# Performance work log

Hardware: AMD Instinct MI355X
Metric: run time of the kernel (lower is better)

## Reference

```python
import jax, jax.numpy as jnp
import numpy as np

NEG_SLOPE = 0.2
EPS = 1e-16


def gatv2_conv(x, src, dst, n_nodes, Wl, Wr, att, bias):
    """GATv2Conv, heads=1, add_self_loops handled by caller via src/dst.
    x: [N, Fin]; src/dst: [E] (message j->i means src=j, dst=i).
    Wl, Wr: [Fin, Fout]; att: [Fout]; bias: [Fout].
    """
    xl = x @ Wl  # [N, Fout] (source transform)
    xr = x @ Wr  # [N, Fout] (target transform)
    # per-edge attention logit: a^T LeakyReLU(xl[j] + xr[i])
    h = xl[src] + xr[dst]                      # [E, Fout]
    e = jax.nn.leaky_relu(h, NEG_SLOPE) @ att  # [E]
    # segment softmax over incoming edges of each dst node
    m = jax.ops.segment_max(e, dst, num_segments=n_nodes)   # [N]
    ex = jnp.exp(e - m[dst])                                 # [E]
    denom = jax.ops.segment_sum(ex, dst, num_segments=n_nodes)  # [N]
    alpha = ex / (denom[dst] + EPS)                          # [E]
    # scatter-aggregate weighted source messages
    out = jax.ops.segment_sum(alpha[:, None] * xl[src], dst, num_segments=n_nodes)
    return out + bias


def glorot(key, shape):
    lim = np.sqrt(6.0 / (shape[0] + shape[1]))
    return jax.random.uniform(key, shape, jnp.float32, -lim, lim)


def setup_inputs() -> dict:
    key = jax.random.key(0)
    ks = jax.random.split(key, 9)
    N, E, Fin, H, Fout = 50000, 800000, 128, 64, 2
    x = jax.random.normal(ks[0], (N, Fin), jnp.float32)
    edge_index = jax.random.randint(ks[1], (2, E), 0, N, jnp.int64)
    return {
        "x": x,
        "edge_index": edge_index,
        "Wl1": glorot(ks[2], (Fin, H)),
        "Wr1": glorot(ks[3], (Fin, H)),
        "att1": glorot(ks[4], (H, 1))[:, 0],
        "b1": jnp.zeros((H,), jnp.float32),
        "Wl2": glorot(ks[5], (H, Fout)),
        "Wr2": glorot(ks[6], (H, Fout)),
        "att2": glorot(ks[7], (Fout, 1))[:, 0],
        "b2": jnp.zeros((Fout,), jnp.float32),
    }


def reference(x, edge_index, Wl1, Wr1, att1, b1, Wl2, Wr2, att2, b2):
    n_nodes = x.shape[0]
    # PyG GATv2Conv adds self-loops by default
    loops = jnp.arange(n_nodes, dtype=edge_index.dtype)
    src = jnp.concatenate([edge_index[0], loops])
    dst = jnp.concatenate([edge_index[1], loops])
    # eval mode: dropout is identity; the initial relu/dropout result is dead code
    h = gatv2_conv(x, src, dst, n_nodes, Wl1, Wr1, att1, b1)
    out = gatv2_conv(h, src, dst, n_nodes, Wl2, Wr2, att2, b2)
    return out
```

## Files before the change

### kernel.cpp

```cpp
#include <hip/hip_runtime.h>
#include <math.h>

#define FIN 128
#define H 64
#define FOUT 2
#define NEG_SLOPE 0.2f
#define EPS 1e-16f

#define SCAN_CHUNK 2048

typedef __attribute__((ext_vector_type(8))) short s8v;
typedef __attribute__((ext_vector_type(4))) float f4v;

__device__ __forceinline__ void load_bs(const int* __restrict__ blocksum, int nscan,
                                        int* bs, int tid){
  if(tid < 64){
    int v = (tid < nscan)? blocksum[tid] : 0;
    int incl = v;
    #pragma unroll
    for(int o=1;o<64;o<<=1){ int u=__shfl_up(incl,o); if(tid>=o) incl+=u; }
    bs[tid] = incl - v;
  }
  __syncthreads();
}

__global__ void k_prep(int* __restrict__ deg, int N, int ZB,
                       const float* __restrict__ Wl, const float* __restrict__ Wr,
                       unsigned short* __restrict__ pWh, unsigned short* __restrict__ pWe){
  int b = blockIdx.x;
  if(b < ZB){
    int i = b*256 + threadIdx.x;
    if(i < N) deg[i] = 0;
    return;
  }
  int idx = (b - ZB)*256 + threadIdx.x;
  int lane = idx & 63;
  int ctk  = idx >> 6;
  int k0   = (ctk & 3) * 32;
  int ct   = ctk >> 2;
  int c    = ct*16 + (lane & 15);
  int kb   = k0 + (lane >> 4)*8;
  const float* Wp = (c < 64) ? (Wl + c) : (Wr + (c - 64));
  #pragma unroll
  for(int j=0;j<8;j++){
    float v = Wp[(size_t)(kb + j)*H];
    unsigned u = __float_as_uint(v);
    unsigned short hb = (unsigned short)(u >> 16);
    float hv = __uint_as_float(((unsigned)hb) << 16);
    float ev = v - hv;
    unsigned short eb = (unsigned short)(__float_as_uint(ev) >> 16);
    pWh[(size_t)idx*8 + j] = hb;
    pWe[(size_t)idx*8 + j] = eb;
  }
}

__global__ __launch_bounds__(256) void k_gemm_deg(
    const float* __restrict__ x,
    const unsigned short* __restrict__ pWh, const unsigned short* __restrict__ pWe,
    float* __restrict__ xl, float* __restrict__ xr,
    unsigned short* __restrict__ xlb, int N, int GG,
    const int* __restrict__ ei, int E, int Etot,
    int* __restrict__ deg, int* __restrict__ rank){
  int tid = threadIdx.x;
  if((int)blockIdx.x >= GG){
    int i0 = (((int)blockIdx.x - GG)*256 + tid)*8;
    if(i0 >= Etot) return;
    if(i0 + 8 <= E && (E & 3) == 0){
      int4 da = *(const int4*)(ei + E + i0);
      int4 db = *(const int4*)(ei + E + i0 + 4);
      int r0 = atomicAdd(&deg[da.x],1);
      int r1 = atomicAdd(&deg[da.y],1);
      int r2 = atomicAdd(&deg[da.z],1);
      int r3 = atomicAdd(&deg[da.w],1);
      int r4 = atomicAdd(&deg[db.x],1);
      int r5 = atomicAdd(&deg[db.y],1);
      int r6 = atomicAdd(&deg[db.z],1);
      int r7 = atomicAdd(&deg[db.w],1);
      *(int4*)(rank + i0)     = make_int4(r0,r1,r2,r3);
      *(int4*)(rank + i0 + 4) = make_int4(r4,r5,r6,r7);
    } else if(i0 >= E && i0 + 8 <= Etot){
      int v = i0 - E;
      int r0 = atomicAdd(&deg[v+0],1);
      int r1 = atomicAdd(&deg[v+1],1);
      int r2 = atomicAdd(&deg[v+2],1);
      int r3 = atomicAdd(&deg[v+3],1);
      int r4 = atomicAdd(&deg[v+4],1);
      int r5 = atomicAdd(&deg[v+5],1);
      int r6 = atomicAdd(&deg[v+6],1);
      int r7 = atomicAdd(&deg[v+7],1);
      *(int4*)(rank + i0)     = make_int4(r0,r1,r2,r3);
      *(int4*)(rank + i0 + 4) = make_int4(r4,r5,r6,r7);
    } else {
      #pragma unroll
      for(int q=0;q<8;q++){
        int i = i0+q; if(i>=Etot) break;
        int dst = (i<E) ? ei[E+i] : (i-E);
        rank[i] = atomicAdd(&deg[dst],1);
      }
    }
    return;
  }

  int lane = tid & 63, wid = tid >> 6;
  int rowbase = blockIdx.x*64 + wid*16;
  int r = lane & 15, g = lane >> 4;

  int arow = rowbase + r; if(arow > N-1) arow = N-1;
  const float* xrow = x + (size_t)arow*FIN;

  s8v ah[4], ae[4];
  #pragma unroll
  for(int k0=0;k0<4;k0++){
    float4 va = *(const float4*)(xrow + k0*32 + g*8);
    float4 vb = *(const float4*)(xrow + k0*32 + g*8 + 4);
    float xs_[8] = {va.x,va.y,va.z,va.w,vb.x,vb.y,vb.z,vb.w};
    #pragma unroll
    for(int j=0;j<8;j++){
      unsigned u = __float_as_uint(xs_[j]);
      unsigned short hb = (unsigned short)(u >> 16);
      ah[k0][j] = (short)hb;
      float ev = xs_[j] - __uint_as_float(((unsigned)hb) << 16);
      ae[k0][j] = (short)(unsigned short)(__float_as_uint(ev) >> 16);
    }
  }

  #pragma unroll 2
  for(int ct=0;ct<8;ct++){
    f4v a = (f4v){0.f,0.f,0.f,0.f};
    #pragma unroll
    for(int k0=0;k0<4;k0++){
      size_t boff = ((size_t)(ct*4 + k0)*64 + lane)*8;
      s8v bh = *(const s8v*)(pWh + boff);
      s8v be = *(const s8v*)(pWe + boff);
      a = __builtin_amdgcn_mfma_f32_16x16x32_bf16(ah[k0], bh, a, 0,0,0);
      a = __builtin_amdgcn_mfma_f32_16x16x32_bf16(ah[k0], be, a, 0,0,0);
      a = __builtin_amdgcn_mfma_f32_16x16x32_bf16(ae[k0], bh, a, 0,0,0);
    }
    float* dst = (ct < 4) ? xl : xr;
    int cc = (ct & 3)*16 + r;
    #pragma unroll
    for(int rr=0;rr<4;rr++){
      int row = rowbase + g*4 + rr;
      if(row < N){
        dst[(size_t)row*H + cc] = a[rr];
        if(ct < 4){
          unsigned u = __float_as_uint(a[rr]);
          xlb[(size_t)row*H + cc] = (unsigned short)((u + 0x7FFF + ((u>>16)&1)) >> 16);
        }
      }
    }
  }
}

__global__ __launch_bounds__(256) void k_scan_a(const int* __restrict__ deg, int n,
                                                int* __restrict__ rowptr,
                                                int* __restrict__ blocksum){
  __shared__ int wsum[4];
  int tid = threadIdx.x, lane = tid & 63, wid = tid >> 6;
  int idx = blockIdx.x*SCAN_CHUNK + tid*8;
  int v[8];
  if(idx + 8 <= n){
    int4 a = *(const int4*)(deg + idx);
    int4 b = *(const int4*)(deg + idx + 4);
    v[0]=a.x;v[1]=a.y;v[2]=a.z;v[3]=a.w;v[4]=b.x;v[5]=b.y;v[6]=b.z;v[7]=b.w;
  } else {
    #pragma unroll
    for(int i=0;i<8;i++) v[i] = (idx+i<n)? deg[idx+i] : 0;
  }
  int pre[8]; int st=0;
  #pragma unroll
  for(int i=0;i<8;i++){ pre[i]=st; st+=v[i]; }
  int incl = st;
  #pragma unroll
  for(int o=1;o<64;o<<=1){ int u=__shfl_up(incl,o); if(lane>=o) incl+=u; }
  if(lane==63) wsum[wid]=incl;
  __syncthreads();
  if(tid==0){ int accu=0; for(int i=0;i<4;i++){ int t=wsum[i]; wsum[i]=accu; accu+=t; } }
  __syncthreads();
  int toff = wsum[wid] + incl - st;
  if(idx + 8 <= n){
    int4 o0 = make_int4(toff+pre[0],toff+pre[1],toff+pre[2],toff+pre[3]);
    int4 o1 = make_int4(toff+pre[4],toff+pre[5],toff+pre[6],toff+pre[7]);
    *(int4*)(rowptr+idx)=o0; *(int4*)(rowptr+idx+4)=o1;
  } else {
    #pragma unroll
    for(int i=0;i<8;i++) if(idx+i<n) rowptr[idx+i]=toff+pre[i];
  }
  if(tid==255){
    blocksum[blockIdx.x] = toff + st;
    if(blockIdx.x == gridDim.x-1) rowptr[n] = toff + st;
  }
}

__global__ void k_fill(const int* __restrict__ ei, int E, int Etot,
                       const int* __restrict__ rowptr,
                       const int* __restrict__ blocksum, int nscan,
                       const int* __restrict__ rank, int* __restrict__ csr_src){
  __shared__ int bs[64];
  int tid = threadIdx.x;
  load_bs(blocksum, nscan, bs, tid);
  int i0 = (blockIdx.x*blockDim.x + tid)*8;
  if(i0 >= Etot) return;
  if(i0 + 8 <= E && (E & 3) == 0){
    int4 sa = *(const int4*)(ei + i0);
    int4 sb = *(const int4*)(ei + i0 + 4);
    int4 da = *(const int4*)(ei + E + i0);
    int4 db = *(const int4*)(ei + E + i0 + 4);
    int4 ra = *(const int4*)(rank + i0);
    int4 rb = *(const int4*)(rank + i0 + 4);
    csr_src[rowptr[da.x] + bs[da.x>>11] + ra.x] = sa.x;
    csr_src[rowptr[da.y] + bs[da.y>>11] + ra.y] = sa.y;
    csr_src[rowptr[da.z] + bs[da.z>>11] + ra.z] = sa.z;
    csr_src[rowptr[da.w] + bs[da.w>>11] + ra.w] = sa.w;
    csr_src[rowptr[db.x] + bs[db.x>>11] + rb.x] = sb.x;
    csr_src[rowptr[db.y] + bs[db.y>>11] + rb.y] = sb.y;
    csr_src[rowptr[db.z] + bs[db.z>>11] + rb.z] = sb.z;
    csr_src[rowptr[db.w] + bs[db.w>>11] + rb.w] = sb.w;
  } else if(i0 >= E && i0 + 8 <= Etot){
    int4 ra = *(const int4*)(rank + i0);
    int4 rb = *(const int4*)(rank + i0 + 4);
    int v = i0 - E;
    csr_src[rowptr[v+0] + bs[(v+0)>>11] + ra.x] = v+0;
    csr_src[rowptr[v+1] + bs[(v+1)>>11] + ra.y] = v+1;
    csr_src[rowptr[v+2] + bs[(v+2)>>11] + ra.z] = v+2;
    csr_src[rowptr[v+3] + bs[(v+3)>>11] + ra.w] = v+3;
    csr_src[rowptr[v+4] + bs[(v+4)>>11] + rb.x] = v+4;
    csr_src[rowptr[v+5] + bs[(v+5)>>11] + rb.y] = v+5;
    csr_src[rowptr[v+6] + bs[(v+6)>>11] + rb.z] = v+6;
    csr_src[rowptr[v+7] + bs[(v+7)>>11] + rb.w] = v+7;
  } else {
    #pragma unroll
    for(int q=0;q<8;q++){
      int i = i0+q; if(i>=Etot) break;
      int src, dst;
      if(i<E){ src = ei[i]; dst = ei[E+i]; } else { src = i-E; dst = i-E; }
      csr_src[rowptr[dst] + bs[dst>>11] + rank[i]] = src;
    }
  }
}

__global__ void k_node1f(const int* __restrict__ rowptr, const int* __restrict__ blocksum,
                         int nscan, const int* __restrict__ csr_src,
                         const unsigned short* __restrict__ xlb, const float* __restrict__ xr,
                         const float* __restrict__ att, const float* __restrict__ b1,
                         const float* __restrict__ Wl2, const float* __restrict__ Wr2,
                         float* __restrict__ xl2, float* __restrict__ xr2, int N){
  __shared__ int bs[64];
  int tid = threadIdx.x;
  load_bs(blocksum, nscan, bs, tid);
  int node = blockIdx.x*8 + (tid>>5);
  int half = (tid >> 4) & 1;
  int gl = tid & 15;
  if(node >= N) return;
  int f4 = gl*4;
  float4 attv = *(const float4*)(att + f4);
  float4 xrv  = *(const float4*)(xr + (size_t)node*H + f4);
  int s = rowptr[node]   + bs[node>>11];
  int t = rowptr[node+1] + bs[(node+1)>>11];
  float d = 0.f;
  float ax=0.f, ay=0.f, az=0.f, aw=0.f;

  for(int k = s + half*8; k < t; k += 16){
    int tl = t - 1;
    int ks[8]; float4 xv[8]; float msk[8];
    #pragma unroll
    for(int j=0;j<8;j++){
      int kj = k + j;
      ks[j] = (kj < t) ? kj : tl;
      msk[j] = (kj < t) ? 1.f : 0.f;
    }
    int ss[8];
    #pragma unroll
    for(int j=0;j<8;j++) ss[j] = csr_src[ks[j]];
    #pragma unroll
    for(int j=0;j<8;j++){
      ushort4 uv = *(const ushort4*)(xlb + (size_t)ss[j]*H + f4);
      xv[j].x = __uint_as_float((unsigned)uv.x << 16);
      xv[j].y = __uint_as_float((unsigned)uv.y << 16);
      xv[j].z = __uint_as_float((unsigned)uv.z << 16);
      xv[j].w = __uint_as_float((unsigned)uv.w << 16);
    }
    #pragma unroll
    for(int j=0;j<8;j++){
      float h0 = xv[j].x + xrv.x, h1 = xv[j].y + xrv.y;
      float h2 = xv[j].z + xrv.z, h3 = xv[j].w + xrv.w;
      float l0 = (h0>0.f)? h0 : NEG_SLOPE*h0;
      float l1 = (h1>0.f)? h1 : NEG_SLOPE*h1;
      float l2 = (h2>0.f)? h2 : NEG_SLOPE*h2;
      float l3 = (h3>0.f)? h3 : NEG_SLOPE*h3;
      float e = l0*attv.x + l1*attv.y + l2*attv.z + l3*attv.w;
      #pragma unroll
      for(int o=1;o<16;o<<=1) e += __shfl_xor(e,o);
      float w = msk[j] * __expf(e);
      d  += w;
      ax += w*xv[j].x; ay += w*xv[j].y; az += w*xv[j].z; aw += w*xv[j].w;
    }
  }

  d  += __shfl_xor(d,16);
  ax += __shfl_xor(ax,16); ay += __shfl_xor(ay,16);
  az += __shfl_xor(az,16); aw += __shfl_xor(aw,16);

  float inv = 1.f/(d + EPS);
  float4 bv = *(const float4*)(b1 + f4);
  float h0 = ax*inv + bv.x, h1 = ay*inv + bv.y;
  float h2 = az*inv + bv.z, h3 = aw*inv + bv.w;
  const float* Wp = half ? Wr2 : Wl2;
  float pa = h0*Wp[(f4+0)*FOUT+0] + h1*Wp[(f4+1)*FOUT+0] + h2*Wp[(f4+2)*FOUT+0] + h3*Wp[(f4+3)*FOUT+0];
  float pb = h0*Wp[(f4+0)*FOUT+1] + h1*Wp[(f4+1)*FOUT+1] + h2*Wp[(f4+2)*FOUT+1] + h3*Wp[(f4+3)*FOUT+1];
  #pragma unroll
  for(int o=1;o<16;o<<=1){
    pa += __shfl_xor(pa,o); pb += __shfl_xor(pb,o);
  }
  if(gl==0){
    float2 pv = make_float2(pa,pb);
    if(half==0) *(float2*)(xl2 + node*2) = pv;
    else        *(float2*)(xr2 + node*2) = pv;
  }
}

__global__ void k_node2(const int* __restrict__ rowptr, const int* __restrict__ blocksum,
                        int nscan, const int* __restrict__ csr_src,
                        const float* __restrict__ xl2, const float* __restrict__ xr2,
                        const float* __restrict__ att2, const float* __restrict__ b2,
                        float* __restrict__ out, int N){
  __shared__ int bs[64];
  int tid = threadIdx.x;
  load_bs(blocksum, nscan, bs, tid);
  int node = blockIdx.x*16 + (tid>>4);
  int gl = tid & 15;
  if(node >= N) return;
  int s = rowptr[node]   + bs[node>>11];
  int t = rowptr[node+1] + bs[(node+1)>>11];
  float2 xrv = *(const float2*)(xr2 + node*2);
  float a0 = att2[0], a1 = att2[1];
  float den=0.f, n0=0.f, n1=0.f;
  for(int k=s+gl; k<t; k+=16){
    int src = csr_src[k];
    float2 xs = *(const float2*)(xl2 + src*2);
    float h0 = xs.x + xrv.x, h1 = xs.y + xrv.y;
    float l0 = (h0>0.f)? h0 : NEG_SLOPE*h0;
    float l1 = (h1>0.f)? h1 : NEG_SLOPE*h1;
    float ex = __expf(l0*a0 + l1*a1);
    den += ex; n0 += ex*xs.x; n1 += ex*xs.y;
  }
  #pragma unroll
  for(int o=1;o<16;o<<=1){
    den += __shfl_xor(den,o);
    n0  += __shfl_xor(n0,o);
    n1  += __shfl_xor(n1,o);
  }
  if(gl==0){
    float inv = 1.f/(den + EPS);
    out[node*2+0] = n0*inv + b2[0];
    out[node*2+1] = n1*inv + b2[1];
  }
}

extern "C" void kernel_launch(void* const* d_in, const int* in_sizes, int n_in,
                              void* d_out, int out_size, void* d_ws, size_t ws_size,
                              hipStream_t stream){
  const float* x    = (const float*)d_in[0];
  const int*   ei   = (const int*)d_in[1];
  const float* Wl1  = (const float*)d_in[2];
  const float* Wr1  = (const float*)d_in[3];
  const float* att1 = (const float*)d_in[4];
  const float* b1   = (const float*)d_in[5];
  const float* Wl2  = (const float*)d_in[6];
  const float* Wr2  = (const float*)d_in[7];
  const float* att2 = (const float*)d_in[8];
  const float* b2   = (const float*)d_in[9];
  int N = in_sizes[0]/FIN;
  int E = in_sizes[1]/2;
  int Etot = E + N;
  int nscan = (N + SCAN_CHUNK - 1) / SCAN_CHUNK;
  int noct  = (Etot + 7) / 8;
  int ZB = (N + 255) / 256;
  int GG = (N + 63) / 64;
  int GDO = (noct + 255) / 256;

  char* w = (char*)d_ws;
  size_t off = 0;
  auto alloc = [&](size_t bytes)->void*{
    void* p = w + off;
    off = (off + bytes + 255) & ~(size_t)255;
    return p;
  };
  float* xl1     = (float*)alloc((size_t)N*H*4);
  float* xr1     = (float*)alloc((size_t)N*H*4);
  unsigned short* xlb = (unsigned short*)alloc((size_t)N*H*2);
  int*   csr_src = (int*)  alloc((size_t)Etot*4);
  int*   rank    = (int*)  alloc((size_t)Etot*4);
  int*   deg     = (int*)  alloc((size_t)N*4);
  int*   rowptr  = (int*)  alloc((size_t)(N+1)*4);
  int*   blocksum= (int*)  alloc((size_t)64*4);
  float* xl2     = (float*)alloc((size_t)N*2*4);
  float* xr2     = (float*)alloc((size_t)N*2*4);
  unsigned short* pWh = (unsigned short*)alloc((size_t)2048*8*2);
  unsigned short* pWe = (unsigned short*)alloc((size_t)2048*8*2);

  k_prep<<<ZB+8, 256, 0, stream>>>(deg, N, ZB, Wl1, Wr1, pWh, pWe);
  k_gemm_deg<<<GG+GDO, 256, 0, stream>>>(x, pWh, pWe, xl1, xr1, xlb, N, GG,
                                         ei, E, Etot, deg, rank);
  k_scan_a<<<nscan,256,0,stream>>>(deg, N, rowptr, blocksum);
  k_fill<<<GDO,256,0,stream>>>(ei, E, Etot, rowptr, blocksum, nscan, rank, csr_src);
  k_node1f<<<(N+7)/8, 256, 0, stream>>>(rowptr, blocksum, nscan, csr_src,
                                        xlb, xr1, att1, b1, Wl2, Wr2, xl2, xr2, N);
  k_node2<<<(N+15)/16, 256, 0, stream>>>(rowptr, blocksum, nscan, csr_src,
                                         xl2, xr2, att2, b2, (float*)d_out, N);
}
```

Before: 122.1 us.

## Split GEMM and degree kernels, drop fp32 xl store, transpose MFMA for vector stores

```diff
diff --git a/kernel.cpp b/kernel.cpp
--- a/kernel.cpp
+++ b/kernel.cpp
@@ -54,61 +54,20 @@
   }
 }
 
-__global__ __launch_bounds__(256) void k_gemm_deg(
+__global__ __launch_bounds__(256) void k_gemm_mfma(
     const float* __restrict__ x,
     const unsigned short* __restrict__ pWh, const unsigned short* __restrict__ pWe,
-    float* __restrict__ xl, float* __restrict__ xr,
-    unsigned short* __restrict__ xlb, int N, int GG,
-    const int* __restrict__ ei, int E, int Etot,
-    int* __restrict__ deg, int* __restrict__ rank){
+    float* __restrict__ xr, unsigned short* __restrict__ xlb, int N){
   int tid = threadIdx.x;
-  if((int)blockIdx.x >= GG){
-    int i0 = (((int)blockIdx.x - GG)*256 + tid)*8;
-    if(i0 >= Etot) return;
-    if(i0 + 8 <= E && (E & 3) == 0){
-      int4 da = *(const int4*)(ei + E + i0);
-      int4 db = *(const int4*)(ei + E + i0 + 4);
-      int r0 = atomicAdd(&deg[da.x],1);
-      int r1 = atomicAdd(&deg[da.y],1);
-      int r2 = atomicAdd(&deg[da.z],1);
-      int r3 = atomicAdd(&deg[da.w],1);
-      int r4 = atomicAdd(&deg[db.x],1);
-      int r5 = atomicAdd(&deg[db.y],1);
-      int r6 = atomicAdd(&deg[db.z],1);
-      int r7 = atomicAdd(&deg[db.w],1);
-      *(int4*)(rank + i0)     = make_int4(r0,r1,r2,r3);
-      *(int4*)(rank + i0 + 4) = make_int4(r4,r5,r6,r7);
-    } else if(i0 >= E && i0 + 8 <= Etot){
-      int v = i0 - E;
-      int r0 = atomicAdd(&deg[v+0],1);
-      int r1 = atomicAdd(&deg[v+1],1);
-      int r2 = atomicAdd(&deg[v+2],1);
-      int r3 = atomicAdd(&deg[v+3],1);
-      int r4 = atomicAdd(&deg[v+4],1);
-      int r5 = atomicAdd(&deg[v+5],1);
-      int r6 = atomicAdd(&deg[v+6],1);
-      int r7 = atomicAdd(&deg[v+7],1);
-      *(int4*)(rank + i0)     = make_int4(r0,r1,r2,r3);
-      *(int4*)(rank + i0 + 4) = make_int4(r4,r5,r6,r7);
-    } else {
-      #pragma unroll
-      for(int q=0;q<8;q++){
-        int i = i0+q; if(i>=Etot) break;
-        int dst = (i<E) ? ei[E+i] : (i-E);
-        rank[i] = atomicAdd(&deg[dst],1);
-      }
-    }
-    return;
-  }
-
   int lane = tid & 63, wid = tid >> 6;
   int rowbase = blockIdx.x*64 + wid*16;
   int r = lane & 15, g = lane >> 4;
 
   int arow = rowbase + r; if(arow > N-1) arow = N-1;
   const float* xrow = x + (size_t)arow*FIN;
-
-  s8v ah[4], ae[4];
+  int orow = rowbase + r;
+
+  s8v xh[4], xe[4];
   #pragma unroll
   for(int k0=0;k0<4;k0++){
     float4 va = *(const float4*)(xrow + k0*32 + g*8);
@@ -118,9 +77,9 @@
     for(int j=0;j<8;j++){
       unsigned u = __float_as_uint(xs_[j]);
       unsigned short hb = (unsigned short)(u >> 16);
-      ah[k0][j] = (short)hb;
+      xh[k0][j] = (short)hb;
       float ev = xs_[j] - __uint_as_float(((unsigned)hb) << 16);
-      ae[k0][j] = (short)(unsigned short)(__float_as_uint(ev) >> 16);
+      xe[k0][j] = (short)(unsigned short)(__float_as_uint(ev) >> 16);
     }
   }
 
@@ -130,24 +89,67 @@
     #pragma unroll
     for(int k0=0;k0<4;k0++){
       size_t boff = ((size_t)(ct*4 + k0)*64 + lane)*8;
-      s8v bh = *(const s8v*)(pWh + boff);
-      s8v be = *(const s8v*)(pWe + boff);
-      a = __builtin_amdgcn_mfma_f32_16x16x32_bf16(ah[k0], bh, a, 0,0,0);
-      a = __builtin_amdgcn_mfma_f32_16x16x32_bf16(ah[k0], be, a, 0,0,0);
-      a = __builtin_amdgcn_mfma_f32_16x16x32_bf16(ae[k0], bh, a, 0,0,0);
-    }
-    float* dst = (ct < 4) ? xl : xr;
-    int cc = (ct & 3)*16 + r;
-    #pragma unroll
-    for(int rr=0;rr<4;rr++){
-      int row = rowbase + g*4 + rr;
-      if(row < N){
-        dst[(size_t)row*H + cc] = a[rr];
-        if(ct < 4){
-          unsigned u = __float_as_uint(a[rr]);
-          xlb[(size_t)row*H + cc] = (unsigned short)((u + 0x7FFF + ((u>>16)&1)) >> 16);
-        }
+      s8v wh = *(const s8v*)(pWh + boff);
+      s8v we = *(const s8v*)(pWe + boff);
+      a = __builtin_amdgcn_mfma_f32_16x16x32_bf16(wh, xh[k0], a, 0,0,0);
+      a = __builtin_amdgcn_mfma_f32_16x16x32_bf16(wh, xe[k0], a, 0,0,0);
+      a = __builtin_amdgcn_mfma_f32_16x16x32_bf16(we, xh[k0], a, 0,0,0);
+    }
+    if(orow < N){
+      if(ct < 4){
+        ushort4 pk;
+        unsigned u0 = __float_as_uint(a[0]);
+        unsigned u1 = __float_as_uint(a[1]);
+        unsigned u2 = __float_as_uint(a[2]);
+        unsigned u3 = __float_as_uint(a[3]);
+        pk.x = (unsigned short)((u0 + 0x7FFF + ((u0>>16)&1)) >> 16);
+        pk.y = (unsigned short)((u1 + 0x7FFF + ((u1>>16)&1)) >> 16);
+        pk.z = (unsigned short)((u2 + 0x7FFF + ((u2>>16)&1)) >> 16);
+        pk.w = (unsigned short)((u3 + 0x7FFF + ((u3>>16)&1)) >> 16);
+        *(ushort4*)(xlb + (size_t)orow*H + ct*16 + g*4) = pk;
+      } else {
+        *(float4*)(xr + (size_t)orow*H + (ct-4)*16 + g*4) =
+            make_float4(a[0],a[1],a[2],a[3]);
       }
+    }
+  }
+}
+
+__global__ void k_degree(const int* __restrict__ ei, int E, int Etot,
+                         int* __restrict__ deg, int* __restrict__ rank){
+  int i0 = (blockIdx.x*blockDim.x + threadIdx.x)*8;
+  if(i0 >= Etot) return;
+  if(i0 + 8 <= E && (E & 3) == 0){
+    int4 da = *(const int4*)(ei + E + i0);
+    int4 db = *(const int4*)(ei + E + i0 + 4);
+    int r0 = atomicAdd(&deg[da.x],1);
+    int r1 = atomicAdd(&deg[da.y],1);
+    int r2 = atomicAdd(&deg[da.z],1);
+    int r3 = atomicAdd(&deg[da.w],1);
+    int r4 = atomicAdd(&deg[db.x],1);
+    int r5 = atomicAdd(&deg[db.y],1);
+    int r6 = atomicAdd(&deg[db.z],1);
+    int r7 = atomicAdd(&deg[db.w],1);
+    *(int4*)(rank + i0)     = make_int4(r0,r1,r2,r3);
+    *(int4*)(rank + i0 + 4) = make_int4(r4,r5,r6,r7);
+  } else if(i0 >= E && i0 + 8 <= Etot){
+    int v = i0 - E;
+    int r0 = atomicAdd(&deg[v+0],1);
+    int r1 = atomicAdd(&deg[v+1],1);
+    int r2 = atomicAdd(&deg[v+2],1);
+    int r3 = atomicAdd(&deg[v+3],1);
+    int r4 = atomicAdd(&deg[v+4],1);
+    int r5 = atomicAdd(&deg[v+5],1);
+    int r6 = atomicAdd(&deg[v+6],1);
+    int r7 = atomicAdd(&deg[v+7],1);
+    *(int4*)(rank + i0)     = make_int4(r0,r1,r2,r3);
+    *(int4*)(rank + i0 + 4) = make_int4(r4,r5,r6,r7);
+  } else {
+    #pragma unroll
+    for(int q=0;q<8;q++){
+      int i = i0+q; if(i>=Etot) break;
+      int dst = (i<E) ? ei[E+i] : (i-E);
+      rank[i] = atomicAdd(&deg[dst],1);
     }
   }
 }
@@ -376,7 +378,6 @@
   int nscan = (N + SCAN_CHUNK - 1) / SCAN_CHUNK;
   int noct  = (Etot + 7) / 8;
   int ZB = (N + 255) / 256;
-  int GG = (N + 63) / 64;
   int GDO = (noct + 255) / 256;
 
   char* w = (char*)d_ws;
@@ -386,7 +387,6 @@
     off = (off + bytes + 255) & ~(size_t)255;
     return p;
   };
-  float* xl1     = (float*)alloc((size_t)N*H*4);
   float* xr1     = (float*)alloc((size_t)N*H*4);
   unsigned short* xlb = (unsigned short*)alloc((size_t)N*H*2);
   int*   csr_src = (int*)  alloc((size_t)Etot*4);
@@ -400,8 +400,8 @@
   unsigned short* pWe = (unsigned short*)alloc((size_t)2048*8*2);
 
   k_prep<<<ZB+8, 256, 0, stream>>>(deg, N, ZB, Wl1, Wr1, pWh, pWe);
-  k_gemm_deg<<<GG+GDO, 256, 0, stream>>>(x, pWh, pWe, xl1, xr1, xlb, N, GG,
-                                         ei, E, Etot, deg, rank);
+  k_gemm_mfma<<<(N+63)/64, 256, 0, stream>>>(x, pWh, pWe, xr1, xlb, N);
+  k_degree<<<GDO,256,0,stream>>>(ei, E, Etot, deg, rank);
   k_scan_a<<<nscan,256,0,stream>>>(deg, N, rowptr, blocksum);
   k_fill<<<GDO,256,0,stream>>>(ei, E, Etot, rowptr, blocksum, nscan, rank, csr_src);
   k_node1f<<<(N+7)/8, 256, 0, stream>>>(rowptr, blocksum, nscan, csr_src,
```

After: 128.8 us. +5.5%, slower.
